# Performance work log

Measured on AMD Instinct MI355X. Metric: run time of the kernel, lower is better.

Reference implementation:

```python
import jax, jax.numpy as jnp
import numpy as np

EPS = 1e-5  # torch LayerNorm default

def setup_inputs() -> dict:
    key = jax.random.key(0)
    k_x, k_w, k_b = jax.random.split(key, 3)
    B, S, D, H = 16, 2048, 2048, 2048
    x = jax.random.normal(k_x, (B, S, D), dtype=jnp.float32)
    # LayerNorm params (torch init: gamma=1, beta=0)
    gamma = jnp.ones((D,), dtype=jnp.float32)
    beta = jnp.zeros((D,), dtype=jnp.float32)
    # Linear params (torch init scale ~ 1/sqrt(D))
    W = jax.random.normal(k_w, (D, H), dtype=jnp.float32) / np.sqrt(D)
    b = jax.random.normal(k_b, (H,), dtype=jnp.float32) / np.sqrt(D)
    return {"x": x, "gamma": gamma, "beta": beta, "W": W, "b": b}

def reference(x, gamma, beta, W, b):
    # LayerNorm over last dim
    mu = jnp.mean(x, axis=-1, keepdims=True)
    var = jnp.mean(jnp.square(x - mu), axis=-1, keepdims=True)
    xn = (x - mu) * jax.lax.rsqrt(var + EPS) * gamma + beta
    # Linear -> exact (erf) GELU, matching torch nn.GELU default
    h = jnp.einsum("bsd,dh->bsh", xn, W) + b
    h = jax.nn.gelu(h, approximate=False)
    # Dropout is identity in eval mode; residual add
    return h + x
```

## Files before the change

kernel.cpp:

```cpp
#include <hip/hip_runtime.h>
#include <math.h>

typedef unsigned short u16;
typedef unsigned int u32;
typedef __attribute__((ext_vector_type(8))) short frag_ab;
typedef __attribute__((ext_vector_type(4))) float floatx4;

__device__ __forceinline__ u16 f2bf(float f){
  u32 u; __builtin_memcpy(&u, &f, 4);
  u32 r = u + 0x7fffu + ((u >> 16) & 1u);
  return (u16)(r >> 16);
}
__device__ __forceinline__ float bf2f(u16 h){
  u32 u = ((u32)h) << 16;
  float f; __builtin_memcpy(&f, &u, 4); return f;
}
__device__ __forceinline__ u32 pack2(float hi, float lo){
  u32 a, b; __builtin_memcpy(&a, &hi, 4); __builtin_memcpy(&b, &lo, 4);
  return __builtin_amdgcn_perm(a, b, 0x07060302u);
}

__device__ __forceinline__ void gload16(u16* l, const u16* g){
  __builtin_amdgcn_global_load_lds(
      (const __attribute__((address_space(1))) void*)g,
      (__attribute__((address_space(3))) void*)l, 16, 0, 0);
}

template<bool XB>
__global__ __launch_bounds__(256) void ln_stats_kernel(
    const float* __restrict__ x, float2* __restrict__ stats,
    u16* __restrict__ xb, int D)
{
  const int row = blockIdx.x;
  const int tid = threadIdx.x;
  const float* xr = x + (size_t)row * D + tid * 8;
  float4 q0 = *(const float4*)xr;
  float4 q1 = *(const float4*)(xr + 4);
  float f[8] = {q0.x,q0.y,q0.z,q0.w,q1.x,q1.y,q1.z,q1.w};
  float s = 0.f, q = 0.f;
#pragma unroll
  for (int i = 0; i < 8; ++i){ s += f[i]; q += f[i]*f[i]; }
#pragma unroll
  for (int o = 32; o > 0; o >>= 1){ s += __shfl_xor(s, o); q += __shfl_xor(q, o); }
  __shared__ float red[2][4];
  const int lane = tid & 63, w = tid >> 6;
  if (lane == 0){ red[0][w] = s; red[1][w] = q; }
  __syncthreads();
  if (XB){
    u16 ov[8];
#pragma unroll
    for (int i = 0; i < 8; ++i) ov[i] = f2bf(f[i]);
    *(uint4*)(xb + (size_t)row * D + tid * 8) = *(const uint4*)ov;
  }
  if (tid == 0){
    float S = red[0][0] + red[0][1] + red[0][2] + red[0][3];
    float Q = red[1][0] + red[1][1] + red[1][2] + red[1][3];
    float invD = 1.0f / (float)D;
    float mu  = S * invD;
    float var = Q * invD - mu * mu;
    stats[row] = make_float2(mu, rsqrtf(var + 1e-5f));
  }
}

__global__ __launch_bounds__(256) void init_uc_kernel(
    const float* __restrict__ b, float* __restrict__ u, float* __restrict__ c, int H)
{
  int t = blockIdx.x * 256 + threadIdx.x;
  if (t < H){ u[t] = 0.f; c[t] = b[t]; }
}

__global__ __launch_bounds__(256) void colsum_kernel(
    const float* __restrict__ W, const float* __restrict__ g, const float* __restrict__ beta,
    float* __restrict__ u, float* __restrict__ c, int D, int H, int KS)
{
  const int n  = blockIdx.x * 256 + threadIdx.x;
  const int k0 = blockIdx.y * KS;
  float su = 0.f, sv = 0.f;
  for (int k = k0; k < k0 + KS; ++k){
    float w = W[(size_t)k * H + n];
    su += g[k] * w;
    sv += beta[k] * w;
  }
  atomicAdd(&u[n], su);
  atomicAdd(&c[n], sv);
}

__global__ __launch_bounds__(256) void transpose_scale_kernel(
    const float* __restrict__ W, const float* __restrict__ g, u16* __restrict__ Wt,
    int D, int H)
{
  __shared__ u16 t[32][33];
  const int bx = blockIdx.x;
  const int by = blockIdx.y;
  const int x = threadIdx.x;
  const int y = threadIdx.y;
#pragma unroll
  for (int i = 0; i < 32; i += 8){
    int k = by * 32 + y + i;
    t[y + i][x] = f2bf(g[k] * W[(size_t)k * H + bx * 32 + x]);
  }
  __syncthreads();
#pragma unroll
  for (int i = 0; i < 32; i += 8)
    Wt[(size_t)(bx * 32 + y + i) * D + by * 32 + x] = t[x][y + i];
}

#define BM 128
#define BN 128
#define BK 32

template<bool XB>
__global__ __launch_bounds__(256) void gemm_kernel(
    const float* __restrict__ Af,
    const u16*   __restrict__ Ab,
    const u16*   __restrict__ B,
    const float2* __restrict__ stats,
    const float* __restrict__ u,
    const float* __restrict__ c,
    float* __restrict__ out,
    int M, int N, int K)
{
  __shared__ __align__(16) u16 As[BM * BK];
  __shared__ __align__(16) u16 Bs[BN * BK];

  const int tid  = threadIdx.x;
  const int lane = tid & 63;
  const int w    = tid >> 6;
  const int wm   = w & 1;
  const int wn   = w >> 1;
  const int lr   = lane & 15;
  const int quad = lane >> 4;
  const int m0 = blockIdx.y * BM;
  const int n0 = blockIdx.x * BN;

  const int r0 = tid >> 2;
  const int c0 = (tid & 3) * 8;
  const u16*   gB0 = B + (size_t)(n0 + r0) * K + c0;
  const u16*   gB1 = gB0 + (size_t)64 * K;
  u16* lA0 = &As[(size_t)tid * 8];
  u16* lA1 = &As[(size_t)(tid + 256) * 8];
  u16* lB0 = &Bs[(size_t)tid * 8];
  u16* lB1 = &Bs[(size_t)(tid + 256) * 8];

  const float* gAf0 = Af + (size_t)(m0 + r0) * K + c0;
  const float* gAf1 = gAf0 + (size_t)64 * K;
  const u16*   gAb0 = Ab + (size_t)(m0 + r0) * K + c0;
  const u16*   gAb1 = gAb0 + (size_t)64 * K;

  floatx4 acc[4][4] = {};

  for (int kt = 0; kt < K; kt += BK){
    uint4 a0, a1;
    if (!XB){
      float4 p0 = *(const float4*)(gAf0 + kt);
      float4 p1 = *(const float4*)(gAf0 + kt + 4);
      float4 p2 = *(const float4*)(gAf1 + kt);
      float4 p3 = *(const float4*)(gAf1 + kt + 4);
      a0.x = pack2(p0.y, p0.x); a0.y = pack2(p0.w, p0.z);
      a0.z = pack2(p1.y, p1.x); a0.w = pack2(p1.w, p1.z);
      a1.x = pack2(p2.y, p2.x); a1.y = pack2(p2.w, p2.z);
      a1.z = pack2(p3.y, p3.x); a1.w = pack2(p3.w, p3.z);
    }

    __syncthreads();
    if (XB){
      gload16(lA0, gAb0 + kt);
      gload16(lA1, gAb1 + kt);
    } else {
      *(uint4*)lA0 = a0; *(uint4*)lA1 = a1;
    }
    gload16(lB0, gB0 + kt);
    gload16(lB1, gB1 + kt);
    __syncthreads();

    frag_ab af[4], bfr[4];
#pragma unroll
    for (int i = 0; i < 4; ++i)
      af[i] = *(const frag_ab*)&As[(wm * 64 + i * 16 + lr) * BK + quad * 8];
#pragma unroll
    for (int j = 0; j < 4; ++j)
      bfr[j] = *(const frag_ab*)&Bs[(wn * 64 + j * 16 + lr) * BK + quad * 8];
#pragma unroll
    for (int i = 0; i < 4; ++i)
#pragma unroll
      for (int j = 0; j < 4; ++j)
        acc[i][j] = __builtin_amdgcn_mfma_f32_16x16x32_bf16(af[i], bfr[j], acc[i][j], 0, 0, 0);
  }

  float uj[4], cj[4];
#pragma unroll
  for (int j = 0; j < 4; ++j){
    const int col = n0 + wn * 64 + j * 16 + lr;
    uj[j] = u[col];
    cj[j] = c[col];
  }
#pragma unroll
  for (int i = 0; i < 4; ++i){
#pragma unroll
    for (int r = 0; r < 4; ++r){
      const int row = m0 + wm * 64 + i * 16 + quad * 4 + r;
      const float2 st = stats[row];
      const float minv = -st.x * st.y;
      float* orow = out + (size_t)row * N;
#pragma unroll
      for (int j = 0; j < 4; ++j){
        const int col = n0 + wn * 64 + j * 16 + lr;
        float vv = st.y * acc[i][j][r] + minv * uj[j] + cj[j];
        float gl = 0.5f * vv * (1.0f + erff(vv * 0.70710678118654752f));
        float res = XB ? bf2f(Ab[(size_t)row * N + col])
                       : Af[(size_t)row * N + col];
        orow[col] = gl + res;
      }
    }
  }
}

extern "C" void kernel_launch(void* const* d_in, const int* in_sizes, int n_in,
                              void* d_out, int out_size, void* d_ws, size_t ws_size,
                              hipStream_t stream) {
  const float* x     = (const float*)d_in[0];
  const float* gamma = (const float*)d_in[1];
  const float* beta  = (const float*)d_in[2];
  const float* W     = (const float*)d_in[3];
  const float* bias  = (const float*)d_in[4];
  float* out = (float*)d_out;

  const int D = in_sizes[1];
  const int H = in_sizes[4];
  const int M = in_sizes[0] / D;

  float2* stats = (float2*)d_ws;
  float*  u     = (float*)(stats + M);
  float*  c     = u + H;
  u16*    Wt    = (u16*)(c + H);
  u16*    xb    = Wt + (size_t)H * D;
  size_t need_base = (size_t)M * 8 + (size_t)H * 8 + (size_t)H * D * 2;
  size_t need_xb   = need_base + (size_t)M * D * 2;
  const bool use_xb = (ws_size >= need_xb);

  if (use_xb)
    ln_stats_kernel<true ><<<M, D / 8, 0, stream>>>(x, stats, xb, D);
  else
    ln_stats_kernel<false><<<M, D / 8, 0, stream>>>(x, stats, xb, D);

  init_uc_kernel<<<(H + 255) / 256, 256, 0, stream>>>(bias, u, c, H);
  const int KS = 128;
  dim3 cg(H / 256, D / KS);
  colsum_kernel<<<cg, 256, 0, stream>>>(W, gamma, beta, u, c, D, H, KS);
  dim3 tb(32, 8), tg(H / 32, D / 32);
  transpose_scale_kernel<<<tg, tb, 0, stream>>>(W, gamma, Wt, D, H);

  dim3 gb(H / BN, M / BM);
  if (use_xb)
    gemm_kernel<true ><<<gb, 256, 0, stream>>>(x, xb, Wt, stats, u, c, out, M, H, D);
  else
    gemm_kernel<false><<<gb, 256, 0, stream>>>(x, xb, Wt, stats, u, c, out, M, H, D);
}
```

Baseline: 972.1 us.

## Double-buffer GEMM LDS tiles, swizzle LDS layout, approximate erf, warp-per-row LN stats

The GEMM main loop now uses two LDS buffers so the next K-tile is staged while MFMAs run on the current one, leaving one barrier per iteration instead of two. LDS rows are XOR-swizzled on both the write and read side to reduce bank conflicts. Exact erff is replaced by an Abramowitz-Stegun polynomial with a fast reciprocal and exp, which cuts epilogue cost but adds error of around 1e-7 in erf. LayerNorm stats now give one wavefront per row, four rows per block, and drop the shared-memory reduction and block barrier.

```diff
diff --git a/kernel.cpp b/kernel.cpp
--- a/kernel.cpp
+++ b/kernel.cpp
@@ -26,38 +26,51 @@
       (__attribute__((address_space(3))) void*)l, 16, 0, 0);
 }
 
+__device__ __forceinline__ float gelu_erf(float v){
+  float z  = v * 0.70710678118654752f;
+  float az = __builtin_fabsf(z);
+  float t  = __builtin_amdgcn_rcpf(__builtin_fmaf(0.3275911f, az, 1.0f));
+  float p  = __builtin_fmaf(t, 1.061405429f, -1.453152027f);
+  p = __builtin_fmaf(p, t, 1.421413741f);
+  p = __builtin_fmaf(p, t, -0.284496736f);
+  p = __builtin_fmaf(p, t, 0.254829592f);
+  p = p * t;
+  float e  = __expf(-az * az);
+  float er = __builtin_fmaf(-p, e, 1.0f);
+  er = copysignf(er, z);
+  return 0.5f * v * (1.0f + er);
+}
+
 template<bool XB>
 __global__ __launch_bounds__(256) void ln_stats_kernel(
     const float* __restrict__ x, float2* __restrict__ stats,
     u16* __restrict__ xb, int D)
 {
-  const int row = blockIdx.x;
-  const int tid = threadIdx.x;
-  const float* xr = x + (size_t)row * D + tid * 8;
-  float4 q0 = *(const float4*)xr;
-  float4 q1 = *(const float4*)(xr + 4);
-  float f[8] = {q0.x,q0.y,q0.z,q0.w,q1.x,q1.y,q1.z,q1.w};
+  const int wid  = threadIdx.x >> 6;
+  const int lane = threadIdx.x & 63;
+  const int row  = blockIdx.x * 4 + wid;
+  const float* xr = x + (size_t)row * D;
+  u16* xbr = xb + (size_t)row * D;
+
   float s = 0.f, q = 0.f;
-#pragma unroll
-  for (int i = 0; i < 8; ++i){ s += f[i]; q += f[i]*f[i]; }
+  for (int base = lane * 4; base < D; base += 256){
+    float4 a = *(const float4*)(xr + base);
+    s += a.x + a.y + a.z + a.w;
+    q = __builtin_fmaf(a.x, a.x, q);
+    q = __builtin_fmaf(a.y, a.y, q);
+    q = __builtin_fmaf(a.z, a.z, q);
+    q = __builtin_fmaf(a.w, a.w, q);
+    if (XB){
+      u16 ov[4] = { f2bf(a.x), f2bf(a.y), f2bf(a.z), f2bf(a.w) };
+      *(uint2*)(xbr + base) = *(const uint2*)ov;
+    }
+  }
 #pragma unroll
   for (int o = 32; o > 0; o >>= 1){ s += __shfl_xor(s, o); q += __shfl_xor(q, o); }
-  __shared__ float red[2][4];
-  const int lane = tid & 63, w = tid >> 6;
-  if (lane == 0){ red[0][w] = s; red[1][w] = q; }
-  __syncthreads();
-  if (XB){
-    u16 ov[8];
-#pragma unroll
-    for (int i = 0; i < 8; ++i) ov[i] = f2bf(f[i]);
-    *(uint4*)(xb + (size_t)row * D + tid * 8) = *(const uint4*)ov;
-  }
-  if (tid == 0){
-    float S = red[0][0] + red[0][1] + red[0][2] + red[0][3];
-    float Q = red[1][0] + red[1][1] + red[1][2] + red[1][3];
+  if (lane == 0){
     float invD = 1.0f / (float)D;
-    float mu  = S * invD;
-    float var = Q * invD - mu * mu;
+    float mu  = s * invD;
+    float var = q * invD - mu * mu;
     stats[row] = make_float2(mu, rsqrtf(var + 1e-5f));
   }
 }
@@ -120,8 +133,8 @@
     float* __restrict__ out,
     int M, int N, int K)
 {
-  __shared__ __align__(16) u16 As[BM * BK];
-  __shared__ __align__(16) u16 Bs[BN * BK];
+  __shared__ __align__(16) u16 As[2][BM * BK];
+  __shared__ __align__(16) u16 Bs[2][BN * BK];
 
   const int tid  = threadIdx.x;
   const int lane = tid & 63;
@@ -134,57 +147,63 @@
   const int n0 = blockIdx.x * BN;
 
   const int r0 = tid >> 2;
-  const int c0 = (tid & 3) * 8;
-  const u16*   gB0 = B + (size_t)(n0 + r0) * K + c0;
-  const u16*   gB1 = gB0 + (size_t)64 * K;
-  u16* lA0 = &As[(size_t)tid * 8];
-  u16* lA1 = &As[(size_t)(tid + 256) * 8];
-  u16* lB0 = &Bs[(size_t)tid * 8];
-  u16* lB1 = &Bs[(size_t)(tid + 256) * 8];
-
-  const float* gAf0 = Af + (size_t)(m0 + r0) * K + c0;
+  const int cs = ((tid & 3) ^ ((r0 >> 1) & 3)) * 8;
+
+  const u16* gB0 = B + (size_t)(n0 + r0) * K + cs;
+  const u16* gB1 = gB0 + (size_t)64 * K;
+  const float* gAf0 = Af + (size_t)(m0 + r0) * K + cs;
   const float* gAf1 = gAf0 + (size_t)64 * K;
-  const u16*   gAb0 = Ab + (size_t)(m0 + r0) * K + c0;
+  const u16*   gAb0 = Ab + (size_t)(m0 + r0) * K + cs;
   const u16*   gAb1 = gAb0 + (size_t)64 * K;
 
+  const int sread = (quad ^ ((lr >> 1) & 3)) * 8;
+
   floatx4 acc[4][4] = {};
-
-  for (int kt = 0; kt < K; kt += BK){
-    uint4 a0, a1;
-    if (!XB){
-      float4 p0 = *(const float4*)(gAf0 + kt);
-      float4 p1 = *(const float4*)(gAf0 + kt + 4);
-      float4 p2 = *(const float4*)(gAf1 + kt);
-      float4 p3 = *(const float4*)(gAf1 + kt + 4);
+  const int NT = K / BK;
+
+  auto stage = [&](int buf, int kt){
+    const int ko = kt * BK;
+    if (XB){
+      gload16(&As[buf][(size_t)tid * 8],         gAb0 + ko);
+      gload16(&As[buf][(size_t)(tid + 256) * 8], gAb1 + ko);
+    } else {
+      float4 p0 = *(const float4*)(gAf0 + ko);
+      float4 p1 = *(const float4*)(gAf0 + ko + 4);
+      float4 p2 = *(const float4*)(gAf1 + ko);
+      float4 p3 = *(const float4*)(gAf1 + ko + 4);
+      uint4 a0, a1;
       a0.x = pack2(p0.y, p0.x); a0.y = pack2(p0.w, p0.z);
       a0.z = pack2(p1.y, p1.x); a0.w = pack2(p1.w, p1.z);
       a1.x = pack2(p2.y, p2.x); a1.y = pack2(p2.w, p2.z);
       a1.z = pack2(p3.y, p3.x); a1.w = pack2(p3.w, p3.z);
+      *(uint4*)&As[buf][(size_t)tid * 8]         = a0;
+      *(uint4*)&As[buf][(size_t)(tid + 256) * 8] = a1;
     }
-
-    __syncthreads();
-    if (XB){
-      gload16(lA0, gAb0 + kt);
-      gload16(lA1, gAb1 + kt);
-    } else {
-      *(uint4*)lA0 = a0; *(uint4*)lA1 = a1;
-    }
-    gload16(lB0, gB0 + kt);
-    gload16(lB1, gB1 + kt);
-    __syncthreads();
+    gload16(&Bs[buf][(size_t)tid * 8],         gB0 + ko);
+    gload16(&Bs[buf][(size_t)(tid + 256) * 8], gB1 + ko);
+  };
+
+  stage(0, 0);
+  __syncthreads();
+
+  for (int kt = 0; kt < NT; ++kt){
+    const int cur = kt & 1;
+    if (kt + 1 < NT) stage(cur ^ 1, kt + 1);
 
     frag_ab af[4], bfr[4];
 #pragma unroll
     for (int i = 0; i < 4; ++i)
-      af[i] = *(const frag_ab*)&As[(wm * 64 + i * 16 + lr) * BK + quad * 8];
+      af[i] = *(const frag_ab*)&As[cur][(wm * 64 + i * 16 + lr) * BK + sread];
 #pragma unroll
     for (int j = 0; j < 4; ++j)
-      bfr[j] = *(const frag_ab*)&Bs[(wn * 64 + j * 16 + lr) * BK + quad * 8];
+      bfr[j] = *(const frag_ab*)&Bs[cur][(wn * 64 + j * 16 + lr) * BK + sread];
 #pragma unroll
     for (int i = 0; i < 4; ++i)
 #pragma unroll
       for (int j = 0; j < 4; ++j)
         acc[i][j] = __builtin_amdgcn_mfma_f32_16x16x32_bf16(af[i], bfr[j], acc[i][j], 0, 0, 0);
+
+    __syncthreads();
   }
 
   float uj[4], cj[4];
@@ -206,7 +225,7 @@
       for (int j = 0; j < 4; ++j){
         const int col = n0 + wn * 64 + j * 16 + lr;
         float vv = st.y * acc[i][j][r] + minv * uj[j] + cj[j];
-        float gl = 0.5f * vv * (1.0f + erff(vv * 0.70710678118654752f));
+        float gl = gelu_erf(vv);
         float res = XB ? bf2f(Ab[(size_t)row * N + col])
                        : Af[(size_t)row * N + col];
         orow[col] = gl + res;
@@ -239,9 +258,9 @@
   const bool use_xb = (ws_size >= need_xb);
 
   if (use_xb)
-    ln_stats_kernel<true ><<<M, D / 8, 0, stream>>>(x, stats, xb, D);
+    ln_stats_kernel<true ><<<M / 4, 256, 0, stream>>>(x, stats, xb, D);
   else
-    ln_stats_kernel<false><<<M, D / 8, 0, stream>>>(x, stats, xb, D);
+    ln_stats_kernel<false><<<M / 4, 256, 0, stream>>>(x, stats, xb, D);
 
   init_uc_kernel<<<(H + 255) / 256, 256, 0, stream>>>(bias, u, c, H);
   const int KS = 128;
```

Measured after the change: 953.3 us. About the same (-1.9%).
